# Performance work log

Measured on AMD Instinct MI355X. Metric: run time of the kernel, lower is better.

## Reference

```python
import jax, jax.numpy as jnp
import numpy as np

B, C, T = 32, 256, 4096

def setup_inputs() -> dict:
    key = jax.random.key(0)
    k1, k2 = jax.random.split(key)
    x = jax.random.normal(k1, (B, C, T), dtype=jnp.float32)
    gamma = jax.random.normal(k2, (1,), dtype=jnp.float32)
    return {"x": x, "gamma": gamma}

def reference(x, gamma):
    # energy[b,i,j] = <x[b,i,:], x[b,j,:]>  -> (B, C, C)
    energy = jnp.einsum('bit,bjt->bij', x, x)
    # max-subtract trick: softmax over (rowmax - energy)
    energy_new = jnp.max(energy, axis=-1, keepdims=True) - energy
    attention = jax.nn.softmax(energy_new, axis=-1)
    # out[b,i,t] = sum_j attention[b,i,j] * x[b,j,t]
    out = jnp.einsum('bij,bjt->bit', attention, x)
    return gamma * out + x
```

## Files before the change

kernel.cpp:

```cpp
#include <hip/hip_runtime.h>
#include <hip/hip_bf16.h>

#define BATCH 32
#define CDIM  256
#define TDIM  4096

using short8  = __attribute__((ext_vector_type(8))) short;
using floatx4 = __attribute__((ext_vector_type(4))) float;

__device__ __forceinline__ unsigned f2bf(float f) {
  unsigned u = __float_as_uint(f);
  return (u + 0x7fffu + ((u >> 16) & 1u)) >> 16;
}
__device__ __forceinline__ unsigned cvt_pk_bf16(float a, float b) {
  return f2bf(a) | (f2bf(b) << 16);
}
__device__ __forceinline__ float bf_lo(unsigned u) { return __uint_as_float(u << 16); }
__device__ __forceinline__ float bf_hi(unsigned u) { return __uint_as_float(u & 0xffff0000u); }

__global__ __launch_bounds__(256, 2)
void gram_kernel(const float* __restrict__ x,
                 float* __restrict__ E1, float* __restrict__ E2) {
  __shared__ __align__(16) short hI[64 * 40];
  __shared__ __align__(16) short lI[64 * 40];
  __shared__ __align__(16) short hJ[64 * 40];

  const int tid = threadIdx.x;
  const int bx  = blockIdx.x;
  const int b   = bx >> 4;
  const int i0  = ((bx >> 2) & 3) * 64;
  const int j0  = (bx & 3) * 64;

  const float* xb = x + ((size_t)b << 20);

  const int srow = tid >> 2;
  const int skq  = (tid & 3) << 3;
  const float* pI = xb + (size_t)(i0 + srow) * TDIM + skq;
  const float* pJ = xb + (size_t)(j0 + srow) * TDIM + skq;

  floatx4 acc_hh[2][2], acc_lh[2][2];
#pragma unroll
  for (int m = 0; m < 2; ++m)
#pragma unroll
    for (int n = 0; n < 2; ++n) {
      acc_hh[m][n] = {0.f, 0.f, 0.f, 0.f};
      acc_lh[m][n] = {0.f, 0.f, 0.f, 0.f};
    }

  const int lane = tid & 63;
  const int w    = tid >> 6;
  const int wm   = (w >> 1) << 5;
  const int wn   = (w & 1) << 5;
  const int fr   = lane & 15;
  const int q    = lane >> 4;

  const int aoff0 = (wm + fr) * 40 + q * 8;
  const int aoff1 = aoff0 + 16 * 40;
  const int boff0 = (wn + fr) * 40 + q * 8;
  const int boff1 = boff0 + 16 * 40;

  float4 rI0 = *(const float4*)pI;
  float4 rI1 = *(const float4*)(pI + 4);
  float4 rJ0 = *(const float4*)pJ;
  float4 rJ1 = *(const float4*)(pJ + 4);

  for (int ks = 0; ks < TDIM / 32; ++ks) {
    unsigned hi01 = cvt_pk_bf16(rI0.x, rI0.y), hi23 = cvt_pk_bf16(rI0.z, rI0.w);
    unsigned hi45 = cvt_pk_bf16(rI1.x, rI1.y), hi67 = cvt_pk_bf16(rI1.z, rI1.w);
    unsigned li01 = cvt_pk_bf16(rI0.x - bf_lo(hi01), rI0.y - bf_hi(hi01));
    unsigned li23 = cvt_pk_bf16(rI0.z - bf_lo(hi23), rI0.w - bf_hi(hi23));
    unsigned li45 = cvt_pk_bf16(rI1.x - bf_lo(hi45), rI1.y - bf_hi(hi45));
    unsigned li67 = cvt_pk_bf16(rI1.z - bf_lo(hi67), rI1.w - bf_hi(hi67));
    unsigned hj01 = cvt_pk_bf16(rJ0.x, rJ0.y), hj23 = cvt_pk_bf16(rJ0.z, rJ0.w);
    unsigned hj45 = cvt_pk_bf16(rJ1.x, rJ1.y), hj67 = cvt_pk_bf16(rJ1.z, rJ1.w);

    __syncthreads();
    *(uint4*)(&hI[srow * 40 + skq]) = make_uint4(hi01, hi23, hi45, hi67);
    *(uint4*)(&lI[srow * 40 + skq]) = make_uint4(li01, li23, li45, li67);
    *(uint4*)(&hJ[srow * 40 + skq]) = make_uint4(hj01, hj23, hj45, hj67);
    __syncthreads();

    if (ks < TDIM / 32 - 1) {
      pI += 32; pJ += 32;
      rI0 = *(const float4*)pI; rI1 = *(const float4*)(pI + 4);
      rJ0 = *(const float4*)pJ; rJ1 = *(const float4*)(pJ + 4);
    }

    short8 Ah0 = *(const short8*)(&hI[aoff0]);
    short8 Ah1 = *(const short8*)(&hI[aoff1]);
    short8 Al0 = *(const short8*)(&lI[aoff0]);
    short8 Al1 = *(const short8*)(&lI[aoff1]);
    short8 Bh0 = *(const short8*)(&hJ[boff0]);
    short8 Bh1 = *(const short8*)(&hJ[boff1]);

    acc_hh[0][0] = __builtin_amdgcn_mfma_f32_16x16x32_bf16(Ah0, Bh0, acc_hh[0][0], 0, 0, 0);
    acc_hh[0][1] = __builtin_amdgcn_mfma_f32_16x16x32_bf16(Ah0, Bh1, acc_hh[0][1], 0, 0, 0);
    acc_hh[1][0] = __builtin_amdgcn_mfma_f32_16x16x32_bf16(Ah1, Bh0, acc_hh[1][0], 0, 0, 0);
    acc_hh[1][1] = __builtin_amdgcn_mfma_f32_16x16x32_bf16(Ah1, Bh1, acc_hh[1][1], 0, 0, 0);
    acc_lh[0][0] = __builtin_amdgcn_mfma_f32_16x16x32_bf16(Al0, Bh0, acc_lh[0][0], 0, 0, 0);
    acc_lh[0][1] = __builtin_amdgcn_mfma_f32_16x16x32_bf16(Al0, Bh1, acc_lh[0][1], 0, 0, 0);
    acc_lh[1][0] = __builtin_amdgcn_mfma_f32_16x16x32_bf16(Al1, Bh0, acc_lh[1][0], 0, 0, 0);
    acc_lh[1][1] = __builtin_amdgcn_mfma_f32_16x16x32_bf16(Al1, Bh1, acc_lh[1][1], 0, 0, 0);
  }

#pragma unroll
  for (int m = 0; m < 2; ++m)
#pragma unroll
    for (int n = 0; n < 2; ++n) {
      const int gr = i0 + wm + 16 * m + 4 * q;
      const int gc = j0 + wn + 16 * n + fr;
      size_t base = (((size_t)b * CDIM + gr) << 8) + gc;
#pragma unroll
      for (int r = 0; r < 4; ++r) {
        E1[base + ((size_t)r << 8)] = acc_hh[m][n][r];
        E2[base + ((size_t)r << 8)] = acc_lh[m][n][r];
      }
    }
}

__global__ __launch_bounds__(256)
void softmax_kernel(const float* __restrict__ E1, const float* __restrict__ E2,
                    __hip_bfloat16* __restrict__ att) {
  const int b = blockIdx.x >> 8;
  const int i = blockIdx.x & 255;
  const int j = threadIdx.x;
  const size_t base = (size_t)b << 16;

  float e = E1[base + (i << 8) + j] + E2[base + (i << 8) + j] + E2[base + (j << 8) + i];
  float z = -e;

  float m = z;
#pragma unroll
  for (int off = 32; off > 0; off >>= 1) m = fmaxf(m, __shfl_xor(m, off, 64));

  __shared__ float red[8];
  const int wv = j >> 6, ln = j & 63;
  if (ln == 0) red[wv] = m;
  __syncthreads();
  m = fmaxf(fmaxf(red[0], red[1]), fmaxf(red[2], red[3]));

  float p = expf(z - m);
  float s = p;
#pragma unroll
  for (int off = 32; off > 0; off >>= 1) s += __shfl_xor(s, off, 64);
  if (ln == 0) red[4 + wv] = s;
  __syncthreads();
  s = (red[4] + red[5]) + (red[6] + red[7]);

  att[base + (i << 8) + j] = __float2bfloat16(p / s);
}

__global__ __launch_bounds__(256, 2)
void pv_kernel(const float* __restrict__ x, const __hip_bfloat16* __restrict__ att,
               const float* __restrict__ gamma, float* __restrict__ out) {
  __shared__ __align__(16) short As[128 * 40];
  __shared__ __align__(16) short Bt[128 * 40];

  const int tid = threadIdx.x;
  const int bx  = blockIdx.x;
  const int b   = bx >> 6;
  const int i0  = ((bx >> 5) & 1) << 7;
  const int t0  = (bx & 31) << 7;

  const float* xb = x + ((size_t)b << 20);
  const unsigned short* attb = (const unsigned short*)att + ((size_t)b << 16);

  const int arow = tid >> 1;
  const int aoff = (tid & 1) << 4;
  const int kg = tid >> 5;
  const int tg = tid & 31;

  floatx4 acc[4][4];
#pragma unroll
  for (int m = 0; m < 4; ++m)
#pragma unroll
    for (int n = 0; n < 4; ++n) acc[m][n] = {0.f, 0.f, 0.f, 0.f};

  const int lane = tid & 63;
  const int w    = tid >> 6;
  const int wm   = (w >> 1) << 6;
  const int wn   = (w & 1) << 6;
  const int fr   = lane & 15;
  const int q    = lane >> 4;

  const unsigned short* pA = attb + (size_t)(i0 + arow) * CDIM + aoff;
  const float* pB = xb + (size_t)(kg * 4) * TDIM + t0 + tg;

  uint4 ra0 = *(const uint4*)pA;
  uint4 ra1 = *(const uint4*)(pA + 8);
  float xv[4][4];
#pragma unroll
  for (int kk = 0; kk < 4; ++kk)
#pragma unroll
    for (int tt = 0; tt < 4; ++tt) xv[kk][tt] = pB[kk * TDIM + tt * 32];

  for (int ks = 0; ks < CDIM / 32; ++ks) {
    unsigned bu[4][2];
#pragma unroll
    for (int tt = 0; tt < 4; ++tt) {
      bu[tt][0] = cvt_pk_bf16(xv[0][tt], xv[1][tt]);
      bu[tt][1] = cvt_pk_bf16(xv[2][tt], xv[3][tt]);
    }

    __syncthreads();
    *(uint4*)(&As[arow * 40 + aoff])     = ra0;
    *(uint4*)(&As[arow * 40 + aoff + 8]) = ra1;
#pragma unroll
    for (int tt = 0; tt < 4; ++tt)
      *(uint2*)(&Bt[(tg + tt * 32) * 40 + kg * 4]) = make_uint2(bu[tt][0], bu[tt][1]);
    __syncthreads();

    if (ks < CDIM / 32 - 1) {
      pA += 32; pB += (size_t)32 * TDIM;
      ra0 = *(const uint4*)pA;
      ra1 = *(const uint4*)(pA + 8);
#pragma unroll
      for (int kk = 0; kk < 4; ++kk)
#pragma unroll
        for (int tt = 0; tt < 4; ++tt) xv[kk][tt] = pB[kk * TDIM + tt * 32];
    }

    short8 Af[4], Bf[4];
#pragma unroll
    for (int m = 0; m < 4; ++m) Af[m] = *(const short8*)(&As[(wm + 16 * m + fr) * 40 + q * 8]);
#pragma unroll
    for (int n = 0; n < 4; ++n) Bf[n] = *(const short8*)(&Bt[(wn + 16 * n + fr) * 40 + q * 8]);
#pragma unroll
    for (int m = 0; m < 4; ++m)
#pragma unroll
      for (int n = 0; n < 4; ++n)
        acc[m][n] = __builtin_amdgcn_mfma_f32_16x16x32_bf16(Af[m], Bf[n], acc[m][n], 0, 0, 0);
  }

  const float g = gamma[0];
#pragma unroll
  for (int m = 0; m < 4; ++m)
#pragma unroll
    for (int n = 0; n < 4; ++n) {
      const int gr = i0 + wm + 16 * m + 4 * q;
      const int gc = t0 + wn + 16 * n + fr;
      size_t base = ((size_t)b << 20) + (size_t)gr * TDIM + gc;
#pragma unroll
      for (int r = 0; r < 4; ++r) {
        size_t idx = base + (size_t)r * TDIM;
        out[idx] = g * acc[m][n][r] + x[idx];
      }
    }
}

extern "C" void kernel_launch(void* const* d_in, const int* in_sizes, int n_in,
                              void* d_out, int out_size, void* d_ws, size_t ws_size,
                              hipStream_t stream) {
  (void)in_sizes; (void)n_in; (void)out_size; (void)ws_size;
  const float* x     = (const float*)d_in[0];
  const float* gamma = (const float*)d_in[1];
  float* out = (float*)d_out;

  const size_t EN = (size_t)BATCH * CDIM * CDIM;
  float* E1 = (float*)d_ws;
  float* E2 = E1 + EN;
  __hip_bfloat16* att = (__hip_bfloat16*)(E2 + EN);

  gram_kernel<<<dim3(512), dim3(256), 0, stream>>>(x, E1, E2);
  softmax_kernel<<<dim3(BATCH * CDIM), dim3(256), 0, stream>>>(E1, E2, att);
  pv_kernel<<<dim3(2048), dim3(256), 0, stream>>>(x, att, gamma, out);
}
```

Before: 413.7 us.

## Enlarge gram tiles with swizzled LDS and batch softmax rows per block

The gram kernel now uses 512-thread blocks with a 128x64 output tile and a 64-wide K step. LDS uses an XOR swizzle instead of padding, and blocks are remapped so co-scheduled blocks share a batch. Half the threads stage the I rows as hi/lo bf16 splits and the other half stage the J rows, which cuts global re-reads of x and the number of barriers. The softmax kernel now handles 32 rows per block and stages the transposed E2 through shared memory, replacing the strided per-element column reads. The cost is lower occupancy (one block per CU, 256 blocks total) and a very uneven load split across threads in the gram stage.

```diff
diff --git a/kernel.cpp b/kernel.cpp
--- a/kernel.cpp
+++ b/kernel.cpp
@@ -18,102 +18,174 @@
 __device__ __forceinline__ float bf_lo(unsigned u) { return __uint_as_float(u << 16); }
 __device__ __forceinline__ float bf_hi(unsigned u) { return __uint_as_float(u & 0xffff0000u); }
 
-__global__ __launch_bounds__(256, 2)
+__global__ __launch_bounds__(512, 1)
 void gram_kernel(const float* __restrict__ x,
                  float* __restrict__ E1, float* __restrict__ E2) {
-  __shared__ __align__(16) short hI[64 * 40];
-  __shared__ __align__(16) short lI[64 * 40];
-  __shared__ __align__(16) short hJ[64 * 40];
+  __shared__ __align__(16) short hI[128 * 64];
+  __shared__ __align__(16) short lI[128 * 64];
+  __shared__ __align__(16) short hJ[64 * 64];
 
   const int tid = threadIdx.x;
   const int bx  = blockIdx.x;
-  const int b   = bx >> 4;
-  const int i0  = ((bx >> 2) & 3) * 64;
-  const int j0  = (bx & 3) * 64;
+
+  const int s   = bx & 7;
+  const int seq = bx >> 3;
+  const int b   = s + ((seq >> 3) << 3);
+  const int job = seq & 7;
+  const int i0  = (job >> 2) << 7;
+  const int j0  = (job & 3) << 6;
 
   const float* xb = x + ((size_t)b << 20);
 
-  const int srow = tid >> 2;
-  const int skq  = (tid & 3) << 3;
-  const float* pI = xb + (size_t)(i0 + srow) * TDIM + skq;
-  const float* pJ = xb + (size_t)(j0 + srow) * TDIM + skq;
-
-  floatx4 acc_hh[2][2], acc_lh[2][2];
+  const bool isJ   = tid >= 256;
+  const int  irow  = tid >> 1;
+  const int  ihalf = tid & 1;
+  const int  jrow  = (tid & 255) >> 2;
+  const int  jq    = tid & 3;
+
+  const float* pS = isJ
+      ? xb + (size_t)(j0 + jrow) * TDIM + (jq << 4)
+      : xb + (size_t)(i0 + irow) * TDIM + (ihalf << 5);
+
+  floatx4 acc1[2][2], acc2[2][2];
 #pragma unroll
   for (int m = 0; m < 2; ++m)
 #pragma unroll
     for (int n = 0; n < 2; ++n) {
-      acc_hh[m][n] = {0.f, 0.f, 0.f, 0.f};
-      acc_lh[m][n] = {0.f, 0.f, 0.f, 0.f};
+      acc1[m][n] = {0.f, 0.f, 0.f, 0.f};
+      acc2[m][n] = {0.f, 0.f, 0.f, 0.f};
     }
 
   const int lane = tid & 63;
   const int w    = tid >> 6;
-  const int wm   = (w >> 1) << 5;
-  const int wn   = (w & 1) << 5;
+  const int wib  = (w >> 1) << 5;
+  const int wjb  = (w & 1) << 5;
   const int fr   = lane & 15;
   const int q    = lane >> 4;
-
-  const int aoff0 = (wm + fr) * 40 + q * 8;
-  const int aoff1 = aoff0 + 16 * 40;
-  const int boff0 = (wn + fr) * 40 + q * 8;
-  const int boff1 = boff0 + 16 * 40;
-
-  float4 rI0 = *(const float4*)pI;
-  float4 rI1 = *(const float4*)(pI + 4);
-  float4 rJ0 = *(const float4*)pJ;
-  float4 rJ1 = *(const float4*)(pJ + 4);
-
-  for (int ks = 0; ks < TDIM / 32; ++ks) {
-    unsigned hi01 = cvt_pk_bf16(rI0.x, rI0.y), hi23 = cvt_pk_bf16(rI0.z, rI0.w);
-    unsigned hi45 = cvt_pk_bf16(rI1.x, rI1.y), hi67 = cvt_pk_bf16(rI1.z, rI1.w);
-    unsigned li01 = cvt_pk_bf16(rI0.x - bf_lo(hi01), rI0.y - bf_hi(hi01));
-    unsigned li23 = cvt_pk_bf16(rI0.z - bf_lo(hi23), rI0.w - bf_hi(hi23));
-    unsigned li45 = cvt_pk_bf16(rI1.x - bf_lo(hi45), rI1.y - bf_hi(hi45));
-    unsigned li67 = cvt_pk_bf16(rI1.z - bf_lo(hi67), rI1.w - bf_hi(hi67));
-    unsigned hj01 = cvt_pk_bf16(rJ0.x, rJ0.y), hj23 = cvt_pk_bf16(rJ0.z, rJ0.w);
-    unsigned hj45 = cvt_pk_bf16(rJ1.x, rJ1.y), hj67 = cvt_pk_bf16(rJ1.z, rJ1.w);
+  const int f7   = fr & 7;
+
+  const int g0 = ((q)     ^ f7) << 3;
+  const int g1 = ((q + 4) ^ f7) << 3;
+  const int a0 = (wib + fr) << 6;
+  const int a1 = (wib + 16 + fr) << 6;
+  const int b0 = (wjb + fr) << 6;
+  const int b1 = (wjb + 16 + fr) << 6;
+
+  float4 r0, r1, r2, r3, r4, r5, r6, r7;
+  r0 = ((const float4*)pS)[0]; r1 = ((const float4*)pS)[1];
+  r2 = ((const float4*)pS)[2]; r3 = ((const float4*)pS)[3];
+  if (!isJ) {
+    r4 = ((const float4*)pS)[4]; r5 = ((const float4*)pS)[5];
+    r6 = ((const float4*)pS)[6]; r7 = ((const float4*)pS)[7];
+  }
+
+  for (int ks = 0; ks < TDIM / 64; ++ks) {
+    unsigned h0 = cvt_pk_bf16(r0.x, r0.y), h1 = cvt_pk_bf16(r0.z, r0.w);
+    unsigned h2 = cvt_pk_bf16(r1.x, r1.y), h3 = cvt_pk_bf16(r1.z, r1.w);
+    unsigned h4 = cvt_pk_bf16(r2.x, r2.y), h5 = cvt_pk_bf16(r2.z, r2.w);
+    unsigned h6 = cvt_pk_bf16(r3.x, r3.y), h7 = cvt_pk_bf16(r3.z, r3.w);
+    unsigned h8, h9, hA, hB, hC, hD, hE, hF;
+    unsigned l0, l1, l2, l3, l4, l5, l6, l7, l8, l9, lA, lB, lC, lD, lE, lF;
+    if (!isJ) {
+      h8 = cvt_pk_bf16(r4.x, r4.y); h9 = cvt_pk_bf16(r4.z, r4.w);
+      hA = cvt_pk_bf16(r5.x, r5.y); hB = cvt_pk_bf16(r5.z, r5.w);
+      hC = cvt_pk_bf16(r6.x, r6.y); hD = cvt_pk_bf16(r6.z, r6.w);
+      hE = cvt_pk_bf16(r7.x, r7.y); hF = cvt_pk_bf16(r7.z, r7.w);
+      l0 = cvt_pk_bf16(r0.x - bf_lo(h0), r0.y - bf_hi(h0));
+      l1 = cvt_pk_bf16(r0.z - bf_lo(h1), r0.w - bf_hi(h1));
+      l2 = cvt_pk_bf16(r1.x - bf_lo(h2), r1.y - bf_hi(h2));
+      l3 = cvt_pk_bf16(r1.z - bf_lo(h3), r1.w - bf_hi(h3));
+      l4 = cvt_pk_bf16(r2.x - bf_lo(h4), r2.y - bf_hi(h4));
+      l5 = cvt_pk_bf16(r2.z - bf_lo(h5), r2.w - bf_hi(h5));
+      l6 = cvt_pk_bf16(r3.x - bf_lo(h6), r3.y - bf_hi(h6));
+      l7 = cvt_pk_bf16(r3.z - bf_lo(h7), r3.w - bf_hi(h7));
+      l8 = cvt_pk_bf16(r4.x - bf_lo(h8), r4.y - bf_hi(h8));
+      l9 = cvt_pk_bf16(r4.z - bf_lo(h9), r4.w - bf_hi(h9));
+      lA = cvt_pk_bf16(r5.x - bf_lo(hA), r5.y - bf_hi(hA));
+      lB = cvt_pk_bf16(r5.z - bf_lo(hB), r5.w - bf_hi(hB));
+      lC = cvt_pk_bf16(r6.x - bf_lo(hC), r6.y - bf_hi(hC));
+      lD = cvt_pk_bf16(r6.z - bf_lo(hD), r6.w - bf_hi(hD));
+      lE = cvt_pk_bf16(r7.x - bf_lo(hE), r7.y - bf_hi(hE));
+      lF = cvt_pk_bf16(r7.z - bf_lo(hF), r7.w - bf_hi(hF));
+    }
 
     __syncthreads();
-    *(uint4*)(&hI[srow * 40 + skq]) = make_uint4(hi01, hi23, hi45, hi67);
-    *(uint4*)(&lI[srow * 40 + skq]) = make_uint4(li01, li23, li45, li67);
-    *(uint4*)(&hJ[srow * 40 + skq]) = make_uint4(hj01, hj23, hj45, hj67);
+    if (!isJ) {
+      const int rb = irow << 6;
+      const int s7 = irow & 7;
+      const int gb = ihalf << 2;
+      *(uint4*)&hI[rb + (((gb + 0) ^ s7) << 3)] = make_uint4(h0, h1, h2, h3);
+      *(uint4*)&hI[rb + (((gb + 1) ^ s7) << 3)] = make_uint4(h4, h5, h6, h7);
+      *(uint4*)&hI[rb + (((gb + 2) ^ s7) << 3)] = make_uint4(h8, h9, hA, hB);
+      *(uint4*)&hI[rb + (((gb + 3) ^ s7) << 3)] = make_uint4(hC, hD, hE, hF);
+      *(uint4*)&lI[rb + (((gb + 0) ^ s7) << 3)] = make_uint4(l0, l1, l2, l3);
+      *(uint4*)&lI[rb + (((gb + 1) ^ s7) << 3)] = make_uint4(l4, l5, l6, l7);
+      *(uint4*)&lI[rb + (((gb + 2) ^ s7) << 3)] = make_uint4(l8, l9, lA, lB);
+      *(uint4*)&lI[rb + (((gb + 3) ^ s7) << 3)] = make_uint4(lC, lD, lE, lF);
+    } else {
+      const int rb = jrow << 6;
+      const int s7 = jrow & 7;
+      const int gb = jq << 1;
+      *(uint4*)&hJ[rb + (((gb + 0) ^ s7) << 3)] = make_uint4(h0, h1, h2, h3);
+      *(uint4*)&hJ[rb + (((gb + 1) ^ s7) << 3)] = make_uint4(h4, h5, h6, h7);
+    }
     __syncthreads();
 
-    if (ks < TDIM / 32 - 1) {
-      pI += 32; pJ += 32;
-      rI0 = *(const float4*)pI; rI1 = *(const float4*)(pI + 4);
-      rJ0 = *(const float4*)pJ; rJ1 = *(const float4*)(pJ + 4);
-    }
-
-    short8 Ah0 = *(const short8*)(&hI[aoff0]);
-    short8 Ah1 = *(const short8*)(&hI[aoff1]);
-    short8 Al0 = *(const short8*)(&lI[aoff0]);
-    short8 Al1 = *(const short8*)(&lI[aoff1]);
-    short8 Bh0 = *(const short8*)(&hJ[boff0]);
-    short8 Bh1 = *(const short8*)(&hJ[boff1]);
-
-    acc_hh[0][0] = __builtin_amdgcn_mfma_f32_16x16x32_bf16(Ah0, Bh0, acc_hh[0][0], 0, 0, 0);
-    acc_hh[0][1] = __builtin_amdgcn_mfma_f32_16x16x32_bf16(Ah0, Bh1, acc_hh[0][1], 0, 0, 0);
-    acc_hh[1][0] = __builtin_amdgcn_mfma_f32_16x16x32_bf16(Ah1, Bh0, acc_hh[1][0], 0, 0, 0);
-    acc_hh[1][1] = __builtin_amdgcn_mfma_f32_16x16x32_bf16(Ah1, Bh1, acc_hh[1][1], 0, 0, 0);
-    acc_lh[0][0] = __builtin_amdgcn_mfma_f32_16x16x32_bf16(Al0, Bh0, acc_lh[0][0], 0, 0, 0);
-    acc_lh[0][1] = __builtin_amdgcn_mfma_f32_16x16x32_bf16(Al0, Bh1, acc_lh[0][1], 0, 0, 0);
-    acc_lh[1][0] = __builtin_amdgcn_mfma_f32_16x16x32_bf16(Al1, Bh0, acc_lh[1][0], 0, 0, 0);
-    acc_lh[1][1] = __builtin_amdgcn_mfma_f32_16x16x32_bf16(Al1, Bh1, acc_lh[1][1], 0, 0, 0);
+    if (ks < TDIM / 64 - 1) {
+      pS += 64;
+      r0 = ((const float4*)pS)[0]; r1 = ((const float4*)pS)[1];
+      r2 = ((const float4*)pS)[2]; r3 = ((const float4*)pS)[3];
+      if (!isJ) {
+        r4 = ((const float4*)pS)[4]; r5 = ((const float4*)pS)[5];
+        r6 = ((const float4*)pS)[6]; r7 = ((const float4*)pS)[7];
+      }
+    }
+
+    {
+      short8 Ah0 = *(const short8*)&hI[a0 + g0];
+      short8 Ah1 = *(const short8*)&hI[a1 + g0];
+      short8 Al0 = *(const short8*)&lI[a0 + g0];
+      short8 Al1 = *(const short8*)&lI[a1 + g0];
+      short8 Bh0 = *(const short8*)&hJ[b0 + g0];
+      short8 Bh1 = *(const short8*)&hJ[b1 + g0];
+      acc1[0][0] = __builtin_amdgcn_mfma_f32_16x16x32_bf16(Ah0, Bh0, acc1[0][0], 0, 0, 0);
+      acc1[0][1] = __builtin_amdgcn_mfma_f32_16x16x32_bf16(Ah0, Bh1, acc1[0][1], 0, 0, 0);
+      acc1[1][0] = __builtin_amdgcn_mfma_f32_16x16x32_bf16(Ah1, Bh0, acc1[1][0], 0, 0, 0);
+      acc1[1][1] = __builtin_amdgcn_mfma_f32_16x16x32_bf16(Ah1, Bh1, acc1[1][1], 0, 0, 0);
+      acc2[0][0] = __builtin_amdgcn_mfma_f32_16x16x32_bf16(Al0, Bh0, acc2[0][0], 0, 0, 0);
+      acc2[0][1] = __builtin_amdgcn_mfma_f32_16x16x32_bf16(Al0, Bh1, acc2[0][1], 0, 0, 0);
+      acc2[1][0] = __builtin_amdgcn_mfma_f32_16x16x32_bf16(Al1, Bh0, acc2[1][0], 0, 0, 0);
+      acc2[1][1] = __builtin_amdgcn_mfma_f32_16x16x32_bf16(Al1, Bh1, acc2[1][1], 0, 0, 0);
+    }
+    {
+      short8 Ah0 = *(const short8*)&hI[a0 + g1];
+      short8 Ah1 = *(const short8*)&hI[a1 + g1];
+      short8 Al0 = *(const short8*)&lI[a0 + g1];
+      short8 Al1 = *(const short8*)&lI[a1 + g1];
+      short8 Bh0 = *(const short8*)&hJ[b0 + g1];
+      short8 Bh1 = *(const short8*)&hJ[b1 + g1];
+      acc1[0][0] = __builtin_amdgcn_mfma_f32_16x16x32_bf16(Ah0, Bh0, acc1[0][0], 0, 0, 0);
+      acc1[0][1] = __builtin_amdgcn_mfma_f32_16x16x32_bf16(Ah0, Bh1, acc1[0][1], 0, 0, 0);
+      acc1[1][0] = __builtin_amdgcn_mfma_f32_16x16x32_bf16(Ah1, Bh0, acc1[1][0], 0, 0, 0);
+      acc1[1][1] = __builtin_amdgcn_mfma_f32_16x16x32_bf16(Ah1, Bh1, acc1[1][1], 0, 0, 0);
+      acc2[0][0] = __builtin_amdgcn_mfma_f32_16x16x32_bf16(Al0, Bh0, acc2[0][0], 0, 0, 0);
+      acc2[0][1] = __builtin_amdgcn_mfma_f32_16x16x32_bf16(Al0, Bh1, acc2[0][1], 0, 0, 0);
+      acc2[1][0] = __builtin_amdgcn_mfma_f32_16x16x32_bf16(Al1, Bh0, acc2[1][0], 0, 0, 0);
+      acc2[1][1] = __builtin_amdgcn_mfma_f32_16x16x32_bf16(Al1, Bh1, acc2[1][1], 0, 0, 0);
+    }
   }
 
 #pragma unroll
   for (int m = 0; m < 2; ++m)
 #pragma unroll
     for (int n = 0; n < 2; ++n) {
-      const int gr = i0 + wm + 16 * m + 4 * q;
-      const int gc = j0 + wn + 16 * n + fr;
+      const int gr = i0 + wib + 16 * m + 4 * q;
+      const int gc = j0 + wjb + 16 * n + fr;
       size_t base = (((size_t)b * CDIM + gr) << 8) + gc;
 #pragma unroll
       for (int r = 0; r < 4; ++r) {
-        E1[base + ((size_t)r << 8)] = acc_hh[m][n][r];
-        E2[base + ((size_t)r << 8)] = acc_lh[m][n][r];
+        E1[base + ((size_t)r << 8)] = acc1[m][n][r];
+        E2[base + ((size_t)r << 8)] = acc2[m][n][r];
       }
     }
 }
@@ -121,33 +193,64 @@
 __global__ __launch_bounds__(256)
 void softmax_kernel(const float* __restrict__ E1, const float* __restrict__ E2,
                     __hip_bfloat16* __restrict__ att) {
-  const int b = blockIdx.x >> 8;
-  const int i = blockIdx.x & 255;
-  const int j = threadIdx.x;
+  __shared__ float SR[32][264];
+  __shared__ float ST[256][33];
+
+  const int tid = threadIdx.x;
+  const int b   = blockIdx.x >> 3;
+  const int i0  = (blockIdx.x & 7) << 5;
   const size_t base = (size_t)b << 16;
 
-  float e = E1[base + (i << 8) + j] + E2[base + (i << 8) + j] + E2[base + (j << 8) + i];
-  float z = -e;
-
-  float m = z;
-#pragma unroll
-  for (int off = 32; off > 0; off >>= 1) m = fmaxf(m, __shfl_xor(m, off, 64));
-
-  __shared__ float red[8];
-  const int wv = j >> 6, ln = j & 63;
-  if (ln == 0) red[wv] = m;
+  {
+    const int r  = tid >> 3;
+    const int c0 = (tid & 7) << 5;
+    const float* p1 = E1 + base + ((size_t)(i0 + r) << 8) + c0;
+    const float* p2 = E2 + base + ((size_t)(i0 + r) << 8) + c0;
+#pragma unroll
+    for (int u = 0; u < 32; u += 4) {
+      float4 a = *(const float4*)(p1 + u);
+      float4 c = *(const float4*)(p2 + u);
+      *(float4*)&SR[r][c0 + u] = make_float4(a.x + c.x, a.y + c.y, a.z + c.z, a.w + c.w);
+    }
+  }
+  {
+    const int c  = tid & 31;
+    const int j0 = (tid >> 5) << 5;
+    const float* p = E2 + base + i0 + c;
+#pragma unroll
+    for (int jj = 0; jj < 32; ++jj)
+      ST[j0 + jj][c] = p[(size_t)(j0 + jj) << 8];
+  }
   __syncthreads();
-  m = fmaxf(fmaxf(red[0], red[1]), fmaxf(red[2], red[3]));
-
-  float p = expf(z - m);
-  float s = p;
-#pragma unroll
-  for (int off = 32; off > 0; off >>= 1) s += __shfl_xor(s, off, 64);
-  if (ln == 0) red[4 + wv] = s;
-  __syncthreads();
-  s = (red[4] + red[5]) + (red[6] + red[7]);
-
-  att[base + (i << 8) + j] = __float2bfloat16(p / s);
+
+  const int r  = tid >> 3;
+  const int t7 = tid & 7;
+  float z[32];
+  float m = -3.4e38f;
+#pragma unroll
+  for (int k = 0; k < 32; ++k) {
+    const int j = t7 + (k << 3);
+    const float e = SR[r][j] + ST[j][r];
+    z[k] = -e;
+    m = fmaxf(m, z[k]);
+  }
+  m = fmaxf(m, __shfl_xor(m, 1, 64));
+  m = fmaxf(m, __shfl_xor(m, 2, 64));
+  m = fmaxf(m, __shfl_xor(m, 4, 64));
+  float ssum = 0.f;
+#pragma unroll
+  for (int k = 0; k < 32; ++k) { z[k] = expf(z[k] - m); ssum += z[k]; }
+  ssum += __shfl_xor(ssum, 1, 64);
+  ssum += __shfl_xor(ssum, 2, 64);
+  ssum += __shfl_xor(ssum, 4, 64);
+  const float inv = 1.f / ssum;
+
+  unsigned short* arow = (unsigned short*)att + base + ((size_t)(i0 + r) << 8);
+#pragma unroll
+  for (int k = 0; k < 32; ++k) {
+    const int j = t7 + (k << 3);
+    arow[j] = (unsigned short)f2bf(z[k] * inv);
+  }
 }
 
 __global__ __launch_bounds__(256, 2)
@@ -261,7 +364,7 @@
   float* E2 = E1 + EN;
   __hip_bfloat16* att = (__hip_bfloat16*)(E2 + EN);
 
-  gram_kernel<<<dim3(512), dim3(256), 0, stream>>>(x, E1, E2);
-  softmax_kernel<<<dim3(BATCH * CDIM), dim3(256), 0, stream>>>(E1, E2, att);
+  gram_kernel<<<dim3(256), dim3(512), 0, stream>>>(x, E1, E2);
+  softmax_kernel<<<dim3(BATCH * 8), dim3(256), 0, stream>>>(E1, E2, att);
   pv_kernel<<<dim3(2048), dim3(256), 0, stream>>>(x, att, gamma, out);
 }
```

After: 408.3 us. No clear change (-1.3%).
